# Performance work log

Measured on AMD Instinct MI355X. Metric: run time of the kernel, lower is better.

## Reference

```python
import jax, jax.numpy as jnp
import numpy as np

B, H, T, D = 2, 8, 2048, 64
STATE = H * D  # 512

def setup_inputs() -> dict:
    key = jax.random.key(0)
    kq, kk, kv, kw, kl = jax.random.split(key, 5)
    q = jax.random.normal(kq, (B * H, T, D), jnp.float32)
    k = jax.random.normal(kk, (B * H, T, D), jnp.float32)
    v = jax.random.normal(kv, (B * H, T, D), jnp.float32)
    # causal position mask: True = masked (future positions)
    position_mask = jnp.triu(jnp.ones((T, T), dtype=bool), 1)
    # per-batch source lengths in [T//2, T]; True = padding (masked)
    lengths = jax.random.randint(kl, (B,), T // 2, T + 1)
    src_length_mask = jnp.arange(T)[None, :] >= lengths[:, None]
    W_merge = jax.random.normal(kw, (STATE, STATE), jnp.float32) / np.sqrt(STATE)
    return {"q": q, "k": k, "v": v, "position_mask": position_mask,
            "src_length_mask": src_length_mask, "W_merge": W_merge}

def reference(q, k, v, position_mask, src_length_mask, W_merge):
    bb, n_dest, d = q.shape              # bb = B*H
    n_batch = src_length_mask.shape[0]
    n_heads = bb // n_batch
    scale = 1.0 / np.sqrt(d)
    # [bb, T_dest, T_src] full score matrix (as in the torch bmm)
    logits = jnp.einsum('btd,bsd->bts', q, k) * scale
    logits = logits.reshape(n_batch, n_heads, n_dest, -1)
    logits = jnp.where(position_mask[None, None], -jnp.inf, logits)
    logits = jnp.where(src_length_mask[:, None, None, :], -jnp.inf, logits)
    scores = jax.nn.softmax(logits, axis=-1).reshape(bb, n_dest, -1)
    # dropout p=0 (eval) -> identity
    out = jnp.einsum('bts,bsd->btd', scores, v)
    out = out.reshape(n_batch, n_heads, n_dest, d).transpose(0, 2, 1, 3)
    out = out.reshape(n_batch, n_dest, n_heads * d)
    return out @ W_merge.T  # bias-free Linear merge
```

## Files before the change

### kernel.cpp

```cpp
#include <hip/hip_runtime.h>

#define TT 2048
#define DD 64
#define NSTATE 512

typedef __attribute__((ext_vector_type(8))) short short8;
typedef __attribute__((ext_vector_type(4))) short short4v;
typedef __attribute__((ext_vector_type(4))) float f4;

__device__ __forceinline__ short f2bf(float x) {
  union { float f; unsigned u; } c; c.f = x;
  unsigned r = (c.u + 0x7FFFu + ((c.u >> 16) & 1u)) >> 16;
  return (short)r;
}

__device__ __forceinline__ bool mask_at(const void* p, bool u8, int idx) {
  return u8 ? (((const unsigned char*)p)[idx] != 0)
            : (((const int*)p)[idx] != 0);
}

__device__ __forceinline__ void gld16(const void* g, void* l) {
  __builtin_amdgcn_global_load_lds(
      (const __attribute__((address_space(1))) void*)g,
      (__attribute__((address_space(3))) void*)l, 16, 0, 0);
}

__global__ __launch_bounds__(256)
void prep_kernel(const float* __restrict__ k, const float* __restrict__ v,
                 const float* __restrict__ W, const void* __restrict__ posmask,
                 const void* __restrict__ srcmask,
                 unsigned short* __restrict__ Wb, unsigned short* __restrict__ Kimg,
                 unsigned short* __restrict__ VTimg, int* __restrict__ lenbuf) {
  const int bidx = blockIdx.x;
  const int tid = threadIdx.x;
  if (bidx < 512) {
    const int bh = bidx >> 5, tile = bidx & 31;
    const float* kp = k + (bh * TT + tile * 64) * DD;
    unsigned short* dst = Kimg + (bh * 32 + tile) * 4096;
#pragma unroll
    for (int t2 = 0; t2 < 2; ++t2) {
      int j = tid + t2 * 256;
      int c8 = j >> 6, r6 = j & 63;
      int kb = c8 >> 1, cc = c8 & 1, qd = r6 >> 4, klo = r6 & 15;
      int key = kb * 16 + klo, dg = cc * 4 + qd;
      f4 a0 = *(const f4*)(kp + key * DD + dg * 8);
      f4 a1 = *(const f4*)(kp + key * DD + dg * 8 + 4);
      short8 o;
      o[0]=f2bf(a0[0]); o[1]=f2bf(a0[1]); o[2]=f2bf(a0[2]); o[3]=f2bf(a0[3]);
      o[4]=f2bf(a1[0]); o[5]=f2bf(a1[1]); o[6]=f2bf(a1[2]); o[7]=f2bf(a1[3]);
      *(short8*)(dst + j * 8) = o;
    }
    __shared__ float Vt[64][65];
    const float* vp = v + (bh * TT + tile * 64) * DD;
    {
      int key = tid >> 2, c0 = (tid & 3) * 16;
#pragma unroll
      for (int i = 0; i < 4; ++i) {
        f4 x = *(const f4*)(vp + key * DD + c0 + i * 4);
        Vt[key][c0 + i * 4 + 0] = x[0];
        Vt[key][c0 + i * 4 + 1] = x[1];
        Vt[key][c0 + i * 4 + 2] = x[2];
        Vt[key][c0 + i * 4 + 3] = x[3];
      }
    }
    __syncthreads();
    unsigned short* vd = VTimg + (bh * 32 + tile) * 4096;
#pragma unroll
    for (int t2 = 0; t2 < 2; ++t2) {
      int cc = tid + t2 * 256;
      int tI = cc >> 5, w5 = cc & 31;
      int dl = w5 >> 1, sg = w5 & 1;
      int db = tI >> 2, sb = tI & 3;
      int d = db * 16 + dl;
      short8 o;
#pragma unroll
      for (int i = 0; i < 8; ++i) o[i] = f2bf(Vt[sb * 16 + sg * 8 + i][d]);
      *(short8*)(vd + tI * 256 + dl * 16 + sg * 8) = o;
    }
  } else if (bidx < 768) {
    int i = ((bidx - 512) * 256 + tid) * 4;
    f4 x = *(const f4*)(W + i);
    short4v o;
    o[0]=f2bf(x[0]); o[1]=f2bf(x[1]); o[2]=f2bf(x[2]); o[3]=f2bf(x[3]);
    *(short4v*)(Wb + i) = o;
  } else {
    const int wv = tid >> 6, lane = tid & 63;
    if (wv < 2) {
      const bool u8 = (((const unsigned char*)posmask)[1] != 0);
      int pos = 1024 + lane * 16;
      bool m1 = mask_at(srcmask, u8, wv * TT + pos);
      unsigned long long bal = __ballot(m1);
      int cur = bal ? (1024 + (__ffsll((unsigned long long)bal) - 1) * 16) : 2048;
      int prev = cur - 16;
      bool m2 = false;
      if (lane < 16) {
        int pos2 = prev + 1 + lane;
        m2 = (pos2 < TT) ? mask_at(srcmask, u8, wv * TT + pos2) : true;
      }
      unsigned long long bal2 = __ballot(m2);
      int len = prev + 1 + (__ffsll((unsigned long long)bal2) - 1);
      if (lane == 0) lenbuf[wv] = len;
    }
  }
}

__global__ __launch_bounds__(128)
void attn_kernel(const float* __restrict__ q, const unsigned short* __restrict__ Kimg,
                 const unsigned short* __restrict__ VTimg,
                 const int* __restrict__ lenbuf,
                 float* __restrict__ Opart, float* __restrict__ lpart) {
  const int bid = blockIdx.x;
  const int chunk = bid >> 10;
  const int rem = bid & 1023;
  const int bh = rem & 15;
  const int qt = rem >> 4;
  const int b = bh >> 3, h = bh & 7; (void)h;
  const int len = lenbuf[b];
  const int n_st = min((qt >> 1) + 1, (len + 63) >> 6);
  const int c0 = chunk * 8;
  if (c0 >= n_st) return;
  const int cend = min(n_st, c0 + 8);

  const int tid = threadIdx.x;
  const int w = tid >> 6, lane = tid & 63;
  const int lane_lo = lane & 15, quad = lane >> 4;
  const int q0 = qt * 32 + w * 16;

  __shared__ __attribute__((aligned(16))) unsigned short Klds[2][4096];
  __shared__ __attribute__((aligned(16))) unsigned short Vlds[2][4096];

  short8 qf[2];
  {
    const float* qrow = q + ((bh * TT) + q0 + lane_lo) * DD;
#pragma unroll
    for (int c = 0; c < 2; ++c) {
      int d0 = c * 32 + quad * 8;
      f4 a0 = *(const f4*)(qrow + d0);
      f4 a1 = *(const f4*)(qrow + d0 + 4);
      short8 t;
      t[0]=f2bf(a0[0]*0.125f); t[1]=f2bf(a0[1]*0.125f);
      t[2]=f2bf(a0[2]*0.125f); t[3]=f2bf(a0[3]*0.125f);
      t[4]=f2bf(a1[0]*0.125f); t[5]=f2bf(a1[1]*0.125f);
      t[6]=f2bf(a1[2]*0.125f); t[7]=f2bf(a1[3]*0.125f);
      qf[c] = t;
    }
  }

  float l_lane = 0.f;
  f4 O[4];
#pragma unroll
  for (int d = 0; d < 4; ++d) O[d] = (f4){0.f, 0.f, 0.f, 0.f};

  const char* kbase = (const char*)(Kimg + (size_t)bh * 32 * 4096);
  const char* vbase = (const char*)(VTimg + (size_t)bh * 32 * 4096);

  auto stage = [&](int st, int bufi) {
    const char* ks = kbase + st * 8192 + w * 4096 + lane * 16;
    char* kl = (char*)&Klds[bufi][0] + w * 4096 + lane * 16;
#pragma unroll
    for (int i = 0; i < 4; ++i) gld16(ks + i * 1024, kl + i * 1024);
    const char* vs = vbase + st * 8192 + w * 4096 + lane * 16;
    char* vl = (char*)&Vlds[bufi][0] + w * 4096 + lane * 16;
#pragma unroll
    for (int i = 0; i < 4; ++i) gld16(vs + i * 1024, vl + i * 1024);
  };

  stage(c0, 0);
  __syncthreads();

  for (int st = c0; st < cend; ++st) {
    const int bufc = (st - c0) & 1;
    if (st + 1 < cend) stage(st + 1, bufc ^ 1);
    const unsigned short* Kl = Klds[bufc];
    const unsigned short* Vl = Vlds[bufc];
    const int s0 = st * 64;

    f4 ST[4];
#pragma unroll
    for (int sb = 0; sb < 4; ++sb) {
      f4 acc = (f4){0.f, 0.f, 0.f, 0.f};
#pragma unroll
      for (int c = 0; c < 2; ++c) {
        short8 kf = *(const short8*)&Kl[((sb * 2 + c) * 64 + lane) * 8];
        acc = __builtin_amdgcn_mfma_f32_16x16x32_bf16(kf, qf[c], acc, 0, 0, 0);
      }
      ST[sb] = acc;
    }

    const bool edge = (st == (qt >> 1)) || (s0 + 64 > len);
    const int tq = q0 + lane_lo;
    short4v pf[4];
#pragma unroll
    for (int sb = 0; sb < 4; ++sb) {
#pragma unroll
      for (int r = 0; r < 4; ++r) {
        float p = __expf(ST[sb][r]);
        if (edge) {
          int s = s0 + sb * 16 + quad * 4 + r;
          if (s > tq || s >= len) p = 0.f;
        }
        l_lane += p;
        pf[sb][r] = f2bf(p);
      }
    }

#pragma unroll
    for (int db = 0; db < 4; ++db) {
      f4 acc = O[db];
#pragma unroll
      for (int sb = 0; sb < 4; ++sb) {
        short4v vf = *(const short4v*)&Vl[(db * 4 + sb) * 256 + lane_lo * 16 + quad * 4];
        acc = __builtin_amdgcn_mfma_f32_16x16x16bf16_1k(pf[sb], vf, acc, 0, 0, 0);
      }
      O[db] = acc;
    }
    __syncthreads();
  }

  l_lane += __shfl_xor(l_lane, 16);
  l_lane += __shfl_xor(l_lane, 32);

  const int pid = (bh << 6) | qt;
  float* ob = Opart + ((size_t)(pid * 4 + chunk)) * 2048;
#pragma unroll
  for (int db = 0; db < 4; ++db)
#pragma unroll
    for (int r = 0; r < 4; ++r)
      ob[(w * 16 + quad * 4 + r) * 64 + db * 16 + lane_lo] = O[db][r];
  if (quad == 0)
    lpart[(pid * 4 + chunk) * 32 + w * 16 + lane_lo] = l_lane;
}

__global__ __launch_bounds__(256)
void combine_kernel(const float* __restrict__ Opart, const float* __restrict__ lpart,
                    const int* __restrict__ lenbuf, unsigned short* __restrict__ merged) {
  const int pid = blockIdx.x;
  const int bh = pid >> 6, qt = pid & 63;
  const int b = bh >> 3, h = bh & 7;
  const int len = lenbuf[b];
  const int n_st = min((qt >> 1) + 1, (len + 63) >> 6);
  const int nch = min(4, (n_st + 7) >> 3);
  const int tid = threadIdx.x;
  const int qi = tid >> 3, dg = tid & 7;
  const float* basep = Opart + (size_t)pid * 4 * 2048 + qi * 64 + dg * 8;
  f4 a0 = (f4){0.f,0.f,0.f,0.f}, a1 = (f4){0.f,0.f,0.f,0.f};
  float l = 0.f;
  for (int ch = 0; ch < nch; ++ch) {
    a0 += *(const f4*)(basep + ch * 2048);
    a1 += *(const f4*)(basep + ch * 2048 + 4);
    l += lpart[(pid * 4 + ch) * 32 + qi];
  }
  float inv = 1.0f / l;
  short8 o;
  o[0]=f2bf(a0[0]*inv); o[1]=f2bf(a0[1]*inv); o[2]=f2bf(a0[2]*inv); o[3]=f2bf(a0[3]*inv);
  o[4]=f2bf(a1[0]*inv); o[5]=f2bf(a1[1]*inv); o[6]=f2bf(a1[2]*inv); o[7]=f2bf(a1[3]*inv);
  *(short8*)&merged[((size_t)(b * TT) + qt * 32 + qi) * NSTATE + h * 64 + dg * 8] = o;
}

__global__ __launch_bounds__(256)
void merge_kernel(const unsigned short* __restrict__ A,
                  const unsigned short* __restrict__ Wb,
                  float* __restrict__ out) {
  __shared__ __attribute__((aligned(16))) unsigned short Wl[64 * 512];
  const int tid = threadIdx.x;
  const int n0 = blockIdx.x * 64, m0 = blockIdx.y * 64;
  {
    int row = tid >> 2, cb = (tid & 3) * 16;
    const unsigned short* src = Wb + (n0 + row) * NSTATE;
#pragma unroll
    for (int j = 0; j < 16; ++j) {
      int c = cb + j;
      int phys = c ^ (row & 7);
      *(short8*)&Wl[row * 512 + phys * 8] = *(const short8*)(src + c * 8);
    }
  }
  __syncthreads();

  const int w = tid >> 6, lane = tid & 63;
  const int lo16 = lane & 15, quad = lane >> 4;
  const int m = m0 + w * 16;
  f4 acc[4];
#pragma unroll
  for (int nf = 0; nf < 4; ++nf) acc[nf] = (f4){0.f, 0.f, 0.f, 0.f};
  const unsigned short* arow = A + (m + lo16) * NSTATE + quad * 8;
#pragma unroll 4
  for (int k0 = 0; k0 < NSTATE; k0 += 32) {
    short8 af = *(const short8*)(arow + k0);
#pragma unroll
    for (int nf = 0; nf < 4; ++nf) {
      int n = nf * 16 + lo16;
      int phys = ((k0 >> 3) + quad) ^ (n & 7);
      short8 bf = *(const short8*)&Wl[n * 512 + phys * 8];
      acc[nf] = __builtin_amdgcn_mfma_f32_16x16x32_bf16(af, bf, acc[nf], 0, 0, 0);
    }
  }
#pragma unroll
  for (int nf = 0; nf < 4; ++nf)
#pragma unroll
    for (int r = 0; r < 4; ++r)
      out[(m + quad * 4 + r) * NSTATE + n0 + nf * 16 + lo16] = acc[nf][r];
}

extern "C" void kernel_launch(void* const* d_in, const int* in_sizes, int n_in,
                              void* d_out, int out_size, void* d_ws, size_t ws_size,
                              hipStream_t stream) {
  (void)in_sizes; (void)n_in; (void)out_size; (void)ws_size;
  const float* q = (const float*)d_in[0];
  const float* k = (const float*)d_in[1];
  const float* v = (const float*)d_in[2];
  const void* posm = d_in[3];
  const void* srcm = d_in[4];
  const float* W = (const float*)d_in[5];
  float* out = (float*)d_out;

  unsigned short* merged = (unsigned short*)d_ws;
  unsigned short* Wb     = merged + 2097152;
  unsigned short* Kimg   = Wb + 262144;
  unsigned short* VTimg  = Kimg + 2097152;
  float* Opart = (float*)(VTimg + 2097152);
  float* lpart = Opart + (size_t)4096 * 2048;
  int* lenbuf  = (int*)(lpart + 4096 * 32);

  prep_kernel<<<dim3(769), dim3(256), 0, stream>>>(k, v, W, posm, srcm,
                                                   Wb, Kimg, VTimg, lenbuf);
  attn_kernel<<<dim3(4096), dim3(128), 0, stream>>>(q, Kimg, VTimg, lenbuf,
                                                    Opart, lpart);
  combine_kernel<<<dim3(1024), dim3(256), 0, stream>>>(Opart, lpart, lenbuf, merged);
  merge_kernel<<<dim3(8, 64), dim3(256), 0, stream>>>(merged, Wb, out);
}
```

Before: 138.7 us.

## Enlarge attention query tiles to 64 and fuse combine with merge projection

The attention kernel now uses 256-thread blocks covering 64 query rows, so each staged K/V tile is shared by four waves instead of two. Split partials are laid out per 64-row tile. The combine and merge kernels become one kernel: each block sums the partial outputs for all heads of 32 query rows, normalizes them, writes a swizzled bf16 tile to LDS, and multiplies it by W read straight from global memory. This drops one launch and the bf16 intermediate round trip. The cost is only 128 merge blocks, fewer attention blocks and less parallelism.

Measured after the change: 159.7 us. +15.1%, slower.

```diff
diff --git a/kernel.cpp b/kernel.cpp
--- a/kernel.cpp
+++ b/kernel.cpp
@@ -104,19 +104,18 @@
   }
 }
 
-__global__ __launch_bounds__(128)
+__global__ __launch_bounds__(256)
 void attn_kernel(const float* __restrict__ q, const unsigned short* __restrict__ Kimg,
                  const unsigned short* __restrict__ VTimg,
                  const int* __restrict__ lenbuf,
                  float* __restrict__ Opart, float* __restrict__ lpart) {
   const int bid = blockIdx.x;
-  const int chunk = bid >> 10;
-  const int rem = bid & 1023;
-  const int bh = rem & 15;
-  const int qt = rem >> 4;
-  const int b = bh >> 3, h = bh & 7; (void)h;
+  const int qt = bid & 31;
+  const int bh = (bid >> 5) & 15;
+  const int chunk = bid >> 9;
+  const int b = bh >> 3;
   const int len = lenbuf[b];
-  const int n_st = min((qt >> 1) + 1, (len + 63) >> 6);
+  const int n_st = min(qt + 1, (len + 63) >> 6);
   const int c0 = chunk * 8;
   if (c0 >= n_st) return;
   const int cend = min(n_st, c0 + 8);
@@ -124,7 +123,7 @@
   const int tid = threadIdx.x;
   const int w = tid >> 6, lane = tid & 63;
   const int lane_lo = lane & 15, quad = lane >> 4;
-  const int q0 = qt * 32 + w * 16;
+  const int q0 = qt * 64 + w * 16;
 
   __shared__ __attribute__((aligned(16))) unsigned short Klds[2][4096];
   __shared__ __attribute__((aligned(16))) unsigned short Vlds[2][4096];
@@ -155,14 +154,14 @@
   const char* vbase = (const char*)(VTimg + (size_t)bh * 32 * 4096);
 
   auto stage = [&](int st, int bufi) {
-    const char* ks = kbase + st * 8192 + w * 4096 + lane * 16;
-    char* kl = (char*)&Klds[bufi][0] + w * 4096 + lane * 16;
-#pragma unroll
-    for (int i = 0; i < 4; ++i) gld16(ks + i * 1024, kl + i * 1024);
-    const char* vs = vbase + st * 8192 + w * 4096 + lane * 16;
-    char* vl = (char*)&Vlds[bufi][0] + w * 4096 + lane * 16;
-#pragma unroll
-    for (int i = 0; i < 4; ++i) gld16(vs + i * 1024, vl + i * 1024);
+    const char* ks = kbase + st * 8192 + w * 2048 + lane * 16;
+    char* kl = (char*)&Klds[bufi][0] + w * 2048 + lane * 16;
+    gld16(ks, kl);
+    gld16(ks + 1024, kl + 1024);
+    const char* vs = vbase + st * 8192 + w * 2048 + lane * 16;
+    char* vl = (char*)&Vlds[bufi][0] + w * 2048 + lane * 16;
+    gld16(vs, vl);
+    gld16(vs + 1024, vl + 1024);
   };
 
   stage(c0, 0);
@@ -187,7 +186,7 @@
       ST[sb] = acc;
     }
 
-    const bool edge = (st == (qt >> 1)) || (s0 + 64 > len);
+    const bool edge = (st == qt) || (s0 + 64 > len);
     const int tq = q0 + lane_lo;
     short4v pf[4];
 #pragma unroll
@@ -220,85 +219,90 @@
   l_lane += __shfl_xor(l_lane, 16);
   l_lane += __shfl_xor(l_lane, 32);
 
-  const int pid = (bh << 6) | qt;
-  float* ob = Opart + ((size_t)(pid * 4 + chunk)) * 2048;
+  const int pid = bh * 32 + qt;
+  float* ob = Opart + (size_t)(pid * 4 + chunk) * 4096;
 #pragma unroll
   for (int db = 0; db < 4; ++db)
 #pragma unroll
     for (int r = 0; r < 4; ++r)
       ob[(w * 16 + quad * 4 + r) * 64 + db * 16 + lane_lo] = O[db][r];
   if (quad == 0)
-    lpart[(pid * 4 + chunk) * 32 + w * 16 + lane_lo] = l_lane;
-}
-
-__global__ __launch_bounds__(256)
-void combine_kernel(const float* __restrict__ Opart, const float* __restrict__ lpart,
-                    const int* __restrict__ lenbuf, unsigned short* __restrict__ merged) {
-  const int pid = blockIdx.x;
-  const int bh = pid >> 6, qt = pid & 63;
-  const int b = bh >> 3, h = bh & 7;
+    lpart[(pid * 4 + chunk) * 64 + w * 16 + lane_lo] = l_lane;
+}
+
+__global__ __launch_bounds__(512)
+void merge_combine_kernel(const float* __restrict__ Opart,
+                          const float* __restrict__ lpart,
+                          const int* __restrict__ lenbuf,
+                          const unsigned short* __restrict__ Wb,
+                          float* __restrict__ out) {
+  __shared__ __attribute__((aligned(16))) unsigned short Al[32 * 512];
+  __shared__ float linv[8][32];
+  const int tid = threadIdx.x;
+  const int b = blockIdx.x >> 6, qt32 = blockIdx.x & 63;
+  const int qt = qt32 >> 1, qoff = (qt32 & 1) * 32;
   const int len = lenbuf[b];
-  const int n_st = min((qt >> 1) + 1, (len + 63) >> 6);
-  const int nch = min(4, (n_st + 7) >> 3);
-  const int tid = threadIdx.x;
-  const int qi = tid >> 3, dg = tid & 7;
-  const float* basep = Opart + (size_t)pid * 4 * 2048 + qi * 64 + dg * 8;
-  f4 a0 = (f4){0.f,0.f,0.f,0.f}, a1 = (f4){0.f,0.f,0.f,0.f};
-  float l = 0.f;
-  for (int ch = 0; ch < nch; ++ch) {
-    a0 += *(const f4*)(basep + ch * 2048);
-    a1 += *(const f4*)(basep + ch * 2048 + 4);
-    l += lpart[(pid * 4 + ch) * 32 + qi];
-  }
-  float inv = 1.0f / l;
-  short8 o;
-  o[0]=f2bf(a0[0]*inv); o[1]=f2bf(a0[1]*inv); o[2]=f2bf(a0[2]*inv); o[3]=f2bf(a0[3]*inv);
-  o[4]=f2bf(a1[0]*inv); o[5]=f2bf(a1[1]*inv); o[6]=f2bf(a1[2]*inv); o[7]=f2bf(a1[3]*inv);
-  *(short8*)&merged[((size_t)(b * TT) + qt * 32 + qi) * NSTATE + h * 64 + dg * 8] = o;
-}
-
-__global__ __launch_bounds__(256)
-void merge_kernel(const unsigned short* __restrict__ A,
-                  const unsigned short* __restrict__ Wb,
-                  float* __restrict__ out) {
-  __shared__ __attribute__((aligned(16))) unsigned short Wl[64 * 512];
-  const int tid = threadIdx.x;
-  const int n0 = blockIdx.x * 64, m0 = blockIdx.y * 64;
+  const int n_st = min(qt + 1, (len + 63) >> 6);
+  const int nch = (n_st + 7) >> 3;
+
+  if (tid < 256) {
+    int h = tid >> 5, ql = tid & 31;
+    int pid = (b * 8 + h) * 32 + qt;
+    float l = 0.f;
+    for (int ch = 0; ch < nch; ++ch)
+      l += lpart[(pid * 4 + ch) * 64 + qoff + ql];
+    linv[h][ql] = 1.0f / l;
+  }
+  __syncthreads();
+
   {
-    int row = tid >> 2, cb = (tid & 3) * 16;
-    const unsigned short* src = Wb + (n0 + row) * NSTATE;
-#pragma unroll
-    for (int j = 0; j < 16; ++j) {
-      int c = cb + j;
-      int phys = c ^ (row & 7);
-      *(short8*)&Wl[row * 512 + phys * 8] = *(const short8*)(src + c * 8);
+    const int hbase = tid >> 8;
+    const int ql = (tid & 255) >> 3;
+    const int d8 = tid & 7;
+#pragma unroll
+    for (int hp = 0; hp < 4; ++hp) {
+      int h = hp * 2 + hbase;
+      int pid = (b * 8 + h) * 32 + qt;
+      const float* basep = Opart + (size_t)(pid * 4) * 4096 + (qoff + ql) * 64 + d8 * 8;
+      f4 a0 = (f4){0.f,0.f,0.f,0.f}, a1 = (f4){0.f,0.f,0.f,0.f};
+      for (int ch = 0; ch < nch; ++ch) {
+        a0 += *(const f4*)(basep + ch * 4096);
+        a1 += *(const f4*)(basep + ch * 4096 + 4);
+      }
+      float inv = linv[h][ql];
+      short8 o;
+      o[0]=f2bf(a0[0]*inv); o[1]=f2bf(a0[1]*inv); o[2]=f2bf(a0[2]*inv); o[3]=f2bf(a0[3]*inv);
+      o[4]=f2bf(a1[0]*inv); o[5]=f2bf(a1[1]*inv); o[6]=f2bf(a1[2]*inv); o[7]=f2bf(a1[3]*inv);
+      int c8 = h * 8 + d8;
+      *(short8*)&Al[ql * 512 + (c8 ^ (ql & 7)) * 8] = o;
     }
   }
   __syncthreads();
 
   const int w = tid >> 6, lane = tid & 63;
   const int lo16 = lane & 15, quad = lane >> 4;
-  const int m = m0 + w * 16;
-  f4 acc[4];
-#pragma unroll
-  for (int nf = 0; nf < 4; ++nf) acc[nf] = (f4){0.f, 0.f, 0.f, 0.f};
-  const unsigned short* arow = A + (m + lo16) * NSTATE + quad * 8;
-#pragma unroll 4
+  const int msub = w & 1, nq = w >> 1;
+  const int row = msub * 16 + lo16;
+  f4 acc[8];
+#pragma unroll
+  for (int nt = 0; nt < 8; ++nt) acc[nt] = (f4){0.f, 0.f, 0.f, 0.f};
+  const unsigned short* wbase = Wb + (nq * 128 + lo16) * NSTATE + quad * 8;
+#pragma unroll
   for (int k0 = 0; k0 < NSTATE; k0 += 32) {
-    short8 af = *(const short8*)(arow + k0);
-#pragma unroll
-    for (int nf = 0; nf < 4; ++nf) {
-      int n = nf * 16 + lo16;
-      int phys = ((k0 >> 3) + quad) ^ (n & 7);
-      short8 bf = *(const short8*)&Wl[n * 512 + phys * 8];
-      acc[nf] = __builtin_amdgcn_mfma_f32_16x16x32_bf16(af, bf, acc[nf], 0, 0, 0);
-    }
-  }
-#pragma unroll
-  for (int nf = 0; nf < 4; ++nf)
+    int c8 = (k0 >> 3) + quad;
+    short8 af = *(const short8*)&Al[row * 512 + (c8 ^ (row & 7)) * 8];
+#pragma unroll
+    for (int nt = 0; nt < 8; ++nt) {
+      short8 bf = *(const short8*)(wbase + nt * 16 * NSTATE + k0);
+      acc[nt] = __builtin_amdgcn_mfma_f32_16x16x32_bf16(af, bf, acc[nt], 0, 0, 0);
+    }
+  }
+  float* orow = out + ((size_t)b * TT + qt32 * 32 + msub * 16) * NSTATE + nq * 128;
+#pragma unroll
+  for (int nt = 0; nt < 8; ++nt)
 #pragma unroll
     for (int r = 0; r < 4; ++r)
-      out[(m + quad * 4 + r) * NSTATE + n0 + nf * 16 + lo16] = acc[nf][r];
+      orow[(quad * 4 + r) * NSTATE + nt * 16 + lo16] = acc[nt][r];
 }
 
 extern "C" void kernel_launch(void* const* d_in, const int* in_sizes, int n_in,
@@ -313,18 +317,17 @@
   const float* W = (const float*)d_in[5];
   float* out = (float*)d_out;
 
-  unsigned short* merged = (unsigned short*)d_ws;
-  unsigned short* Wb     = merged + 2097152;
-  unsigned short* Kimg   = Wb + 262144;
-  unsigned short* VTimg  = Kimg + 2097152;
+  unsigned short* Wb    = (unsigned short*)d_ws;
+  unsigned short* Kimg  = Wb + 262144;
+  unsigned short* VTimg = Kimg + 2097152;
   float* Opart = (float*)(VTimg + 2097152);
-  float* lpart = Opart + (size_t)4096 * 2048;
-  int* lenbuf  = (int*)(lpart + 4096 * 32);
+  float* lpart = Opart + (size_t)512 * 4 * 4096;
+  int* lenbuf  = (int*)(lpart + 512 * 4 * 64);
 
   prep_kernel<<<dim3(769), dim3(256), 0, stream>>>(k, v, W, posm, srcm,
                                                    Wb, Kimg, VTimg, lenbuf);
-  attn_kernel<<<dim3(4096), dim3(128), 0, stream>>>(q, Kimg, VTimg, lenbuf,
+  attn_kernel<<<dim3(2048), dim3(256), 0, stream>>>(q, Kimg, VTimg, lenbuf,
                                                     Opart, lpart);
-  combine_kernel<<<dim3(1024), dim3(256), 0, stream>>>(Opart, lpart, lenbuf, merged);
-  merge_kernel<<<dim3(8, 64), dim3(256), 0, stream>>>(merged, Wb, out);
-}
+  merge_combine_kernel<<<dim3(128), dim3(512), 0, stream>>>(Opart, lpart, lenbuf,
+                                                            Wb, out);
+}
```

## Replace LDS-staged attention with per-wave register-fed K/V loads and 32-query waves

Applied to the files above, without the earlier changes.

The attention kernel drops shared-memory double buffering and block barriers. Each wave now handles 32 query rows on its own, loading K and V fragments straight from global memory into registers and prefetching the next K tile. The V image layout in prep is changed to match the register fragment order, and split-K chunking goes from 8 to 4 key tiles with up to 8 partial outputs per row. This removes LDS traffic and syncs and reuses each K/V fragment across two query sub-tiles, at the cost of more registers, more partial-sum traffic in combine, and reliance on L2 for K/V reuse across waves.

After: 140.1 us. About the same (+1.0%).

```diff
diff --git a/kernel.cpp b/kernel.cpp
--- a/kernel.cpp
+++ b/kernel.cpp
@@ -17,12 +17,6 @@
 __device__ __forceinline__ bool mask_at(const void* p, bool u8, int idx) {
   return u8 ? (((const unsigned char*)p)[idx] != 0)
             : (((const int*)p)[idx] != 0);
-}
-
-__device__ __forceinline__ void gld16(const void* g, void* l) {
-  __builtin_amdgcn_global_load_lds(
-      (const __attribute__((address_space(1))) void*)g,
-      (__attribute__((address_space(3))) void*)l, 16, 0, 0);
 }
 
 __global__ __launch_bounds__(256)
@@ -30,7 +24,7 @@
                  const float* __restrict__ W, const void* __restrict__ posmask,
                  const void* __restrict__ srcmask,
                  unsigned short* __restrict__ Wb, unsigned short* __restrict__ Kimg,
-                 unsigned short* __restrict__ VTimg, int* __restrict__ lenbuf) {
+                 unsigned short* __restrict__ Vimg, int* __restrict__ lenbuf) {
   const int bidx = blockIdx.x;
   const int tid = threadIdx.x;
   if (bidx < 512) {
@@ -64,18 +58,21 @@
       }
     }
     __syncthreads();
-    unsigned short* vd = VTimg + (bh * 32 + tile) * 4096;
+    unsigned short* vd = Vimg + (bh * 32 + tile) * 4096;
 #pragma unroll
     for (int t2 = 0; t2 < 2; ++t2) {
       int cc = tid + t2 * 256;
-      int tI = cc >> 5, w5 = cc & 31;
-      int dl = w5 >> 1, sg = w5 & 1;
-      int db = tI >> 2, sb = tI & 3;
-      int d = db * 16 + dl;
+      int gI = cc >> 6, ln = cc & 63;
+      int llo = ln & 15, qd = ln >> 4;
+      int db = gI >> 1, sbp = gI & 1;
+      int d = db * 16 + llo, sA = sbp * 32 + qd * 4;
       short8 o;
 #pragma unroll
-      for (int i = 0; i < 8; ++i) o[i] = f2bf(Vt[sb * 16 + sg * 8 + i][d]);
-      *(short8*)(vd + tI * 256 + dl * 16 + sg * 8) = o;
+      for (int j = 0; j < 4; ++j) {
+        o[j]     = f2bf(Vt[sA + j][d]);
+        o[4 + j] = f2bf(Vt[sA + 16 + j][d]);
+      }
+      *(short8*)(vd + gI * 512 + ln * 8) = o;
     }
   } else if (bidx < 768) {
     int i = ((bidx - 512) * 256 + tid) * 4;
@@ -104,157 +101,164 @@
   }
 }
 
-__global__ __launch_bounds__(128)
+__global__ __launch_bounds__(256)
 void attn_kernel(const float* __restrict__ q, const unsigned short* __restrict__ Kimg,
-                 const unsigned short* __restrict__ VTimg,
+                 const unsigned short* __restrict__ Vimg,
                  const int* __restrict__ lenbuf,
                  float* __restrict__ Opart, float* __restrict__ lpart) {
-  const int bid = blockIdx.x;
-  const int chunk = bid >> 10;
-  const int rem = bid & 1023;
-  const int bh = rem & 15;
-  const int qt = rem >> 4;
-  const int b = bh >> 3, h = bh & 7; (void)h;
+  const int g = blockIdx.x * 4 + (threadIdx.x >> 6);
+  const int chunk = g >> 10;
+  const int rem = g & 1023;
+  const int bh = rem >> 6;
+  const int qw = rem & 63;
+  const int b = bh >> 3;
   const int len = lenbuf[b];
-  const int n_st = min((qt >> 1) + 1, (len + 63) >> 6);
-  const int c0 = chunk * 8;
+  const int n_st = min((qw >> 1) + 1, (len + 63) >> 6);
+  const int c0 = chunk * 4;
   if (c0 >= n_st) return;
-  const int cend = min(n_st, c0 + 8);
-
-  const int tid = threadIdx.x;
-  const int w = tid >> 6, lane = tid & 63;
+  const int cend = min(n_st, c0 + 4);
+
+  const int lane = threadIdx.x & 63;
   const int lane_lo = lane & 15, quad = lane >> 4;
-  const int q0 = qt * 32 + w * 16;
-
-  __shared__ __attribute__((aligned(16))) unsigned short Klds[2][4096];
-  __shared__ __attribute__((aligned(16))) unsigned short Vlds[2][4096];
-
-  short8 qf[2];
+  const int q0 = qw * 32;
+
+  short8 qf[2][2];
   {
-    const float* qrow = q + ((bh * TT) + q0 + lane_lo) * DD;
-#pragma unroll
-    for (int c = 0; c < 2; ++c) {
-      int d0 = c * 32 + quad * 8;
-      f4 a0 = *(const f4*)(qrow + d0);
-      f4 a1 = *(const f4*)(qrow + d0 + 4);
-      short8 t;
-      t[0]=f2bf(a0[0]*0.125f); t[1]=f2bf(a0[1]*0.125f);
-      t[2]=f2bf(a0[2]*0.125f); t[3]=f2bf(a0[3]*0.125f);
-      t[4]=f2bf(a1[0]*0.125f); t[5]=f2bf(a1[1]*0.125f);
-      t[6]=f2bf(a1[2]*0.125f); t[7]=f2bf(a1[3]*0.125f);
-      qf[c] = t;
-    }
-  }
-
-  float l_lane = 0.f;
-  f4 O[4];
-#pragma unroll
-  for (int d = 0; d < 4; ++d) O[d] = (f4){0.f, 0.f, 0.f, 0.f};
-
-  const char* kbase = (const char*)(Kimg + (size_t)bh * 32 * 4096);
-  const char* vbase = (const char*)(VTimg + (size_t)bh * 32 * 4096);
-
-  auto stage = [&](int st, int bufi) {
-    const char* ks = kbase + st * 8192 + w * 4096 + lane * 16;
-    char* kl = (char*)&Klds[bufi][0] + w * 4096 + lane * 16;
-#pragma unroll
-    for (int i = 0; i < 4; ++i) gld16(ks + i * 1024, kl + i * 1024);
-    const char* vs = vbase + st * 8192 + w * 4096 + lane * 16;
-    char* vl = (char*)&Vlds[bufi][0] + w * 4096 + lane * 16;
-#pragma unroll
-    for (int i = 0; i < 4; ++i) gld16(vs + i * 1024, vl + i * 1024);
-  };
-
-  stage(c0, 0);
-  __syncthreads();
+    const float* qbase = q + ((size_t)bh * TT + q0 + lane_lo) * DD;
+#pragma unroll
+    for (int qi = 0; qi < 2; ++qi)
+#pragma unroll
+      for (int c = 0; c < 2; ++c) {
+        const float* r = qbase + qi * 16 * DD + c * 32 + quad * 8;
+        f4 a0 = *(const f4*)r;
+        f4 a1 = *(const f4*)(r + 4);
+        short8 t;
+        t[0]=f2bf(a0[0]*0.125f); t[1]=f2bf(a0[1]*0.125f);
+        t[2]=f2bf(a0[2]*0.125f); t[3]=f2bf(a0[3]*0.125f);
+        t[4]=f2bf(a1[0]*0.125f); t[5]=f2bf(a1[1]*0.125f);
+        t[6]=f2bf(a1[2]*0.125f); t[7]=f2bf(a1[3]*0.125f);
+        qf[qi][c] = t;
+      }
+  }
+
+  const short8* Kb = (const short8*)(Kimg + (size_t)bh * 32 * 4096);
+  const short8* Vb = (const short8*)(Vimg + (size_t)bh * 32 * 4096);
+
+  float l0 = 0.f, l1 = 0.f;
+  f4 O[2][4];
+#pragma unroll
+  for (int qi = 0; qi < 2; ++qi)
+#pragma unroll
+    for (int d = 0; d < 4; ++d) O[qi][d] = (f4){0.f, 0.f, 0.f, 0.f};
+
+  short8 kf[8], kn[8], vv[8];
+  {
+    const short8* kp = Kb + c0 * 512 + lane;
+#pragma unroll
+    for (int i = 0; i < 8; ++i) kf[i] = kp[i * 64];
+  }
 
   for (int st = c0; st < cend; ++st) {
-    const int bufc = (st - c0) & 1;
-    if (st + 1 < cend) stage(st + 1, bufc ^ 1);
-    const unsigned short* Kl = Klds[bufc];
-    const unsigned short* Vl = Vlds[bufc];
+    const short8* vp = Vb + st * 512 + lane;
+#pragma unroll
+    for (int i = 0; i < 8; ++i) vv[i] = vp[i * 64];
+    if (st + 1 < cend) {
+      const short8* kp = Kb + (st + 1) * 512 + lane;
+#pragma unroll
+      for (int i = 0; i < 8; ++i) kn[i] = kp[i * 64];
+    }
+
+    f4 ST[2][4];
+#pragma unroll
+    for (int sb = 0; sb < 4; ++sb)
+#pragma unroll
+      for (int qi = 0; qi < 2; ++qi) {
+        f4 acc = (f4){0.f, 0.f, 0.f, 0.f};
+        acc = __builtin_amdgcn_mfma_f32_16x16x32_bf16(kf[sb * 2 + 0], qf[qi][0], acc, 0, 0, 0);
+        acc = __builtin_amdgcn_mfma_f32_16x16x32_bf16(kf[sb * 2 + 1], qf[qi][1], acc, 0, 0, 0);
+        ST[qi][sb] = acc;
+      }
+
     const int s0 = st * 64;
-
-    f4 ST[4];
-#pragma unroll
-    for (int sb = 0; sb < 4; ++sb) {
-      f4 acc = (f4){0.f, 0.f, 0.f, 0.f};
-#pragma unroll
-      for (int c = 0; c < 2; ++c) {
-        short8 kf = *(const short8*)&Kl[((sb * 2 + c) * 64 + lane) * 8];
-        acc = __builtin_amdgcn_mfma_f32_16x16x32_bf16(kf, qf[c], acc, 0, 0, 0);
-      }
-      ST[sb] = acc;
-    }
-
-    const bool edge = (st == (qt >> 1)) || (s0 + 64 > len);
-    const int tq = q0 + lane_lo;
-    short4v pf[4];
-#pragma unroll
-    for (int sb = 0; sb < 4; ++sb) {
-#pragma unroll
-      for (int r = 0; r < 4; ++r) {
-        float p = __expf(ST[sb][r]);
-        if (edge) {
-          int s = s0 + sb * 16 + quad * 4 + r;
-          if (s > tq || s >= len) p = 0.f;
+    const bool edge = (s0 + 63 > q0) || (s0 + 64 > len);
+    short4v pf[2][4];
+#pragma unroll
+    for (int qi = 0; qi < 2; ++qi) {
+      const int tq = q0 + qi * 16 + lane_lo;
+#pragma unroll
+      for (int sb = 0; sb < 4; ++sb)
+#pragma unroll
+        for (int r = 0; r < 4; ++r) {
+          float p = __expf(ST[qi][sb][r]);
+          if (edge) {
+            int s = s0 + sb * 16 + quad * 4 + r;
+            if (s > tq || s >= len) p = 0.f;
+          }
+          if (qi) l1 += p; else l0 += p;
+          pf[qi][sb][r] = f2bf(p);
         }
-        l_lane += p;
-        pf[sb][r] = f2bf(p);
-      }
-    }
-
-#pragma unroll
-    for (int db = 0; db < 4; ++db) {
-      f4 acc = O[db];
+    }
+
+#pragma unroll
+    for (int db = 0; db < 4; ++db)
 #pragma unroll
       for (int sb = 0; sb < 4; ++sb) {
-        short4v vf = *(const short4v*)&Vl[(db * 4 + sb) * 256 + lane_lo * 16 + quad * 4];
-        acc = __builtin_amdgcn_mfma_f32_16x16x16bf16_1k(pf[sb], vf, acc, 0, 0, 0);
-      }
-      O[db] = acc;
-    }
-    __syncthreads();
-  }
-
-  l_lane += __shfl_xor(l_lane, 16);
-  l_lane += __shfl_xor(l_lane, 32);
-
-  const int pid = (bh << 6) | qt;
-  float* ob = Opart + ((size_t)(pid * 4 + chunk)) * 2048;
-#pragma unroll
-  for (int db = 0; db < 4; ++db)
-#pragma unroll
-    for (int r = 0; r < 4; ++r)
-      ob[(w * 16 + quad * 4 + r) * 64 + db * 16 + lane_lo] = O[db][r];
-  if (quad == 0)
-    lpart[(pid * 4 + chunk) * 32 + w * 16 + lane_lo] = l_lane;
+        short8 v8 = vv[db * 2 + (sb >> 1)];
+        short4v vf = (sb & 1) ? __builtin_shufflevector(v8, v8, 4, 5, 6, 7)
+                              : __builtin_shufflevector(v8, v8, 0, 1, 2, 3);
+#pragma unroll
+        for (int qi = 0; qi < 2; ++qi)
+          O[qi][db] = __builtin_amdgcn_mfma_f32_16x16x16bf16_1k(pf[qi][sb], vf, O[qi][db], 0, 0, 0);
+      }
+
+    if (st + 1 < cend) {
+#pragma unroll
+      for (int i = 0; i < 8; ++i) kf[i] = kn[i];
+    }
+  }
+
+  l0 += __shfl_xor(l0, 16); l0 += __shfl_xor(l0, 32);
+  l1 += __shfl_xor(l1, 16); l1 += __shfl_xor(l1, 32);
+
+  const int pid = bh * 64 + qw;
+  float* ob = Opart + (size_t)(pid * 8 + chunk) * 2048;
+#pragma unroll
+  for (int qi = 0; qi < 2; ++qi)
+#pragma unroll
+    for (int db = 0; db < 4; ++db)
+#pragma unroll
+      for (int r = 0; r < 4; ++r)
+        ob[(qi * 16 + quad * 4 + r) * 64 + db * 16 + lane_lo] = O[qi][db][r];
+  if (quad == 0) {
+    lpart[(pid * 8 + chunk) * 32 + lane_lo] = l0;
+    lpart[(pid * 8 + chunk) * 32 + 16 + lane_lo] = l1;
+  }
 }
 
 __global__ __launch_bounds__(256)
 void combine_kernel(const float* __restrict__ Opart, const float* __restrict__ lpart,
                     const int* __restrict__ lenbuf, unsigned short* __restrict__ merged) {
   const int pid = blockIdx.x;
-  const int bh = pid >> 6, qt = pid & 63;
+  const int bh = pid >> 6, qw = pid & 63;
   const int b = bh >> 3, h = bh & 7;
   const int len = lenbuf[b];
-  const int n_st = min((qt >> 1) + 1, (len + 63) >> 6);
-  const int nch = min(4, (n_st + 7) >> 3);
+  const int n_st = min((qw >> 1) + 1, (len + 63) >> 6);
+  const int nch = (n_st + 3) >> 2;
   const int tid = threadIdx.x;
   const int qi = tid >> 3, dg = tid & 7;
-  const float* basep = Opart + (size_t)pid * 4 * 2048 + qi * 64 + dg * 8;
+  const float* basep = Opart + (size_t)pid * 8 * 2048 + qi * 64 + dg * 8;
   f4 a0 = (f4){0.f,0.f,0.f,0.f}, a1 = (f4){0.f,0.f,0.f,0.f};
   float l = 0.f;
   for (int ch = 0; ch < nch; ++ch) {
     a0 += *(const f4*)(basep + ch * 2048);
     a1 += *(const f4*)(basep + ch * 2048 + 4);
-    l += lpart[(pid * 4 + ch) * 32 + qi];
+    l += lpart[(pid * 8 + ch) * 32 + qi];
   }
   float inv = 1.0f / l;
   short8 o;
   o[0]=f2bf(a0[0]*inv); o[1]=f2bf(a0[1]*inv); o[2]=f2bf(a0[2]*inv); o[3]=f2bf(a0[3]*inv);
   o[4]=f2bf(a1[0]*inv); o[5]=f2bf(a1[1]*inv); o[6]=f2bf(a1[2]*inv); o[7]=f2bf(a1[3]*inv);
-  *(short8*)&merged[((size_t)(b * TT) + qt * 32 + qi) * NSTATE + h * 64 + dg * 8] = o;
+  *(short8*)&merged[((size_t)(b * TT) + qw * 32 + qi) * NSTATE + h * 64 + dg * 8] = o;
 }
 
 __global__ __launch_bounds__(256)
@@ -313,17 +317,17 @@
   const float* W = (const float*)d_in[5];
   float* out = (float*)d_out;
 
-  unsigned short* merged = (unsigned short*)d_ws;
-  unsigned short* Wb     = merged + 2097152;
+  unsigned short* Wb     = (unsigned short*)d_ws;
   unsigned short* Kimg   = Wb + 262144;
-  unsigned short* VTimg  = Kimg + 2097152;
-  float* Opart = (float*)(VTimg + 2097152);
-  float* lpart = Opart + (size_t)4096 * 2048;
-  int* lenbuf  = (int*)(lpart + 4096 * 32);
+  unsigned short* Vimg   = Kimg + 2097152;
+  unsigned short* merged = Vimg + 2097152;
+  float* Opart = (float*)(merged + 2097152);
+  float* lpart = Opart + (size_t)1024 * 8 * 2048;
+  int* lenbuf  = (int*)(lpart + 1024 * 8 * 32);
 
   prep_kernel<<<dim3(769), dim3(256), 0, stream>>>(k, v, W, posm, srcm,
-                                                   Wb, Kimg, VTimg, lenbuf);
-  attn_kernel<<<dim3(4096), dim3(128), 0, stream>>>(q, Kimg, VTimg, lenbuf,
+                                                   Wb, Kimg, Vimg, lenbuf);
+  attn_kernel<<<dim3(2048), dim3(256), 0, stream>>>(q, Kimg, Vimg, lenbuf,
                                                     Opart, lpart);
   combine_kernel<<<dim3(1024), dim3(256), 0, stream>>>(Opart, lpart, lenbuf, merged);
   merge_kernel<<<dim3(8, 64), dim3(256), 0, stream>>>(merged, Wb, out);
```
